# Kernel optimization log

Measured on AMD Instinct MI355X. Metric: run time of the kernel, lower is better.

The kernel has to match this reference:

```python
import jax, jax.numpy as jnp
from jax import lax
import numpy as np

KERNEL_SIZE = 29
N_T = 1000
SIGMA_MIN, SIGMA_MAX = 0.5, 20.0
HIDDEN = 32


def _gaussian_kernel1d(sigma, ksize):
    # torchvision: linspace over [-half, half], normalized gaussian pdf
    half = (ksize - 1) * 0.5
    xg = jnp.linspace(-half, half, ksize)
    pdf = jnp.exp(-0.5 * (xg / sigma) ** 2)
    return pdf / pdf.sum()


def batch_blur(x, sigmas, ksize=KERNEL_SIZE):
    # x: [B,C,H,W], sigmas: [B]. Per-sample separable gaussian blur as a single
    # grouped depthwise conv (feature_group_count = B*C) instead of a Python loop.
    B, C, H, W = x.shape
    k1 = jax.vmap(lambda s: _gaussian_kernel1d(s, ksize))(sigmas)  # [B, k]
    pad = ksize // 2
    xp = jnp.pad(x, ((0, 0), (0, 0), (pad, pad), (pad, pad)), mode='reflect')
    lhs = xp.reshape(1, B * C, H + 2 * pad, W + 2 * pad)
    kbc = jnp.repeat(k1, C, axis=0)  # [B*C, k] per-channel kernel
    # vertical pass then horizontal pass (outer-product 2D kernel == two 1D passes)
    y = lax.conv_general_dilated(lhs, kbc[:, None, :, None], (1, 1), 'VALID',
                                 feature_group_count=B * C)
    y = lax.conv_general_dilated(y, kbc[:, None, None, :], (1, 1), 'VALID',
                                 feature_group_count=B * C)
    return y.reshape(B, C, H, W)


def gt_net(z, tn, W1, b1, tw, W2, b2):
    # simple time-conditioned conv net standing in for the opaque `gt` module
    h = lax.conv_general_dilated(z, W1, (1, 1), 'SAME')  # [B,HIDDEN,H,W]
    h = h + b1[None, :, None, None] + (tn[:, None] * tw[None, :])[:, :, None, None]
    h = jax.nn.relu(h)
    out = lax.conv_general_dilated(h, W2, (1, 1), 'SAME') + b2[None, :, None, None]
    return out


def setup_inputs() -> dict:
    key = jax.random.key(0)
    ks = jax.random.split(key, 6)
    B, C, H, W = 32, 3, 256, 256
    x = jax.random.normal(ks[0], (B, C, H, W), dtype=jnp.float32)
    t = jax.random.randint(ks[1], (B,), 0, N_T, dtype=jnp.int32)
    W1 = jax.random.normal(ks[2], (HIDDEN, C, 3, 3), dtype=jnp.float32) * 0.1
    b1 = jnp.zeros((HIDDEN,), dtype=jnp.float32)
    tw = jax.random.normal(ks[3], (HIDDEN,), dtype=jnp.float32) * 0.1
    W2 = jax.random.normal(ks[4], (C, HIDDEN, 3, 3), dtype=jnp.float32) * 0.1
    b2 = jnp.zeros((C,), dtype=jnp.float32)
    sigma_schedule = jnp.linspace(SIGMA_MIN, SIGMA_MAX, N_T, dtype=jnp.float32)
    return {"x": x, "t": t, "W1": W1, "b1": b1, "tw": tw, "W2": W2, "b2": b2,
            "sigma_schedule": sigma_schedule}


def reference(x, t, W1, b1, tw, W2, b2, sigma_schedule):
    sigma_t = sigma_schedule[t]                      # [B]
    z_t = batch_blur(x, sigma_t, KERNEL_SIZE)        # [B,C,H,W]
    preds = gt_net(z_t, t.astype(jnp.float32) / N_T, W1, b1, tw, W2, b2)
    return jnp.mean((x - preds) ** 2)                # MSELoss
```

## Files before the change

### kernel.cpp

```cpp
#include <hip/hip_runtime.h>
#include <hip/hip_bf16.h>

#define BATCH 32
#define CH 3
#define HH 256
#define WW 256
#define KS 29
#define PAD 14
#define NT_F 1000.0f

#define RB 16

typedef __attribute__((ext_vector_type(8))) short short8;
typedef __attribute__((ext_vector_type(4))) float f32x4;
typedef __attribute__((ext_vector_type(16))) float f32x16;

union U4 { short8 s8; uint4 u4; };

__device__ inline unsigned short bf16rne(float f) {
  unsigned u = __float_as_uint(f);
  unsigned r = (u + 0x7FFFu + ((u >> 16) & 1u)) >> 16;
  return (unsigned short)r;
}
__device__ inline unsigned pk_bf16(float a, float b) {
  union { __hip_bfloat162 h2; unsigned u; } cv;
  cv.h2 = __float22bfloat162_rn(make_float2(a, b));
  return cv.u;
}


#define PARTIAL_OFF 3151872

__global__ __launch_bounds__(256, 4) void blur_kernel(
    const float* __restrict__ x, const int* __restrict__ t,
    const float* __restrict__ sched, const float* __restrict__ W1,
    const float* __restrict__ b1, const float* __restrict__ tw,
    const float* __restrict__ W2, float* __restrict__ ws,
    unsigned short* __restrict__ z) {
  int blk = blockIdx.x;
  int tid = threadIdx.x;

  if (blk >= BATCH * CH * RB) {
    float* tcond = ws + 1024;
    unsigned short* w1n = (unsigned short*)(ws + 2048);
    unsigned short* w2c = (unsigned short*)(ws + 2816);
    for (int i = tid; i < 1536; i += 256) {
      int mf = i >> 9, r = i & 511;
      int och = r >> 4, s = r & 15;
      int tp = mf * 4 + (s >> 2), ci = s & 3;
      w1n[i] = (ci < 3 && tp < 9) ? bf16rne(W1[och * 27 + ci * 9 + tp])
                                  : (unsigned short)0;
    }
    for (int i = tid; i < 4608; i += 256) {
      int tap = i >> 9, r = i & 511;
      int n = r >> 5, s = r & 31;
      int och = (s & 3) + 8 * ((s >> 2) & 3) + 4 * (s >> 4);
      int dy = tap / 3, dx = tap - dy * 3;
      w2c[i] = (n < 3) ? bf16rne(W2[((n * 32 + och) * 3 + dy) * 3 + dx])
                       : (unsigned short)0;
    }
    for (int i = tid; i < 1024; i += 256) {
      int b = i >> 5, o = i & 31;
      tcond[i] = b1[o] + ((float)t[b] * (1.0f / NT_F)) * tw[o];
    }
    return;
  }

  {
    int wid = (blk & 7) * 192 + (blk >> 3);
    blk = wid;
  }

  __shared__ float vsp[RB][288];
  __shared__ float gkl[32];
  int rg = blk & (RB - 1);
  int bc = blk >> 4;
  int b = bc / CH;
  int y0 = rg * RB;
  const float* xp = x + (size_t)bc * (HH * WW);

  if (tid < 64) {
    float wexp = 0.0f;
    if (tid < KS) {
      float sigma = sched[t[b]];
      float xg = (float)(tid - PAD) / sigma;
      wexp = expf(-0.5f * xg * xg);
    }
    float s = wexp;
#pragma unroll
    for (int off = 32; off > 0; off >>= 1) s += __shfl_down(s, off);
    float tot = __shfl(s, 0);
    if (tid < 32) gkl[tid] = wexp / tot;
  }
  __syncthreads();

  float gk[KS];
#pragma unroll
  for (int kk = 0; kk < KS; kk++) gk[kk] = gkl[kk];

#pragma unroll
  for (int ch = 0; ch < 2; ch++) {
    float acc[8];
#pragma unroll
    for (int yy = 0; yy < 8; yy++) acc[yy] = 0.0f;
#pragma unroll
    for (int i = 0; i < 36; i++) {
      int gy = y0 + 8 * ch - PAD + i;
      gy = (gy < 0) ? -gy : gy;
      gy = (gy >= HH) ? (2 * HH - 2 - gy) : gy;
      float v = xp[gy * WW + tid];
#pragma unroll
      for (int yy = 0; yy < 8; yy++) {
        int kk = i - yy;
        if (kk >= 0 && kk < KS) acc[yy] += gk[kk] * v;
      }
    }
#pragma unroll
    for (int yy = 0; yy < 8; yy++) vsp[8 * ch + yy][tid + 16] = acc[yy];
  }
  __syncthreads();
  {
    int row = tid >> 4, i2 = tid & 15;
    vsp[row][i2] = vsp[row][32 - i2];
    vsp[row][272 + i2] = vsp[row][270 - i2];
  }
  __syncthreads();

  size_t zb = (size_t)bc * (HH * WW);
#pragma unroll
  for (int it = 0; it < RB / 4; ++it) {
    int unit = tid + 256 * it;
    int row = unit >> 6, cg = unit & 63;
    float w[36];
#pragma unroll
    for (int i = 0; i < 9; i++)
      *(float4*)&w[4 * i] = *(const float4*)&vsp[row][4 * (cg + i)];
    float o0 = 0, o1 = 0, o2 = 0, o3 = 0;
#pragma unroll
    for (int kk = 0; kk < KS; kk++) {
      float kv = gk[kk];
      o0 += kv * w[2 + kk];
      o1 += kv * w[3 + kk];
      o2 += kv * w[4 + kk];
      o3 += kv * w[5 + kk];
    }
    unsigned u0 = pk_bf16(o0, o1);
    unsigned u1 = pk_bf16(o2, o3);
    *(uint2*)&z[zb + (size_t)(y0 + row) * WW + 4 * cg] = make_uint2(u0, u1);
  }
}

__global__ __launch_bounds__(256, 5) void convloss_kernel(
    const float* __restrict__ x, const float* __restrict__ ws,
    const float* __restrict__ b2g, float* __restrict__ partial) {
  __shared__ __align__(16) unsigned short zs4[400 * 4];
  __shared__ __align__(16) unsigned short hsw[4 * 6 * 18 * 32];
  __shared__ float wsum[4];

  const float* tcond = ws + 1024;
  const unsigned short* w1n = (const unsigned short*)(ws + 2048);
  const unsigned short* w2c = (const unsigned short*)(ws + 2816);
  const unsigned short* zg = (const unsigned short*)(ws + 5120);

  int flat = (blockIdx.z * 16 + blockIdx.y) * 16 + blockIdx.x;
  int wid = (flat & 7) * 1024 + (flat >> 3);
  int b = wid >> 8;
  int by = (wid >> 4) & 15;
  int bx = wid & 15;

  int tid = threadIdx.x;
  int x0 = bx * 16, y0 = by * 16;
  const unsigned short* zbp = zg + (size_t)b * 3 * HH * WW;

  int lane = tid & 63;
  int q = lane >> 4;
  int col = lane & 15;
  int col32 = lane & 31;
  int h = lane >> 5;
  int wv = tid >> 6;

  if (tid < 200) {
    int zy = tid / 10;
    int zx2 = tid - zy * 10;
    int gy = y0 - 2 + zy;
    int gx0 = x0 - 2 + 2 * zx2;
    bool ok = ((unsigned)gy < (unsigned)HH) && ((unsigned)gx0 < (unsigned)(WW - 1));
    int cy = (gy < 0) ? 0 : ((gy > 255) ? 255 : gy);
    int cx = (gx0 < 0) ? 0 : ((gx0 > 254) ? 254 : gx0);
    int gi = cy * WW + cx;
    unsigned c0 = *(const unsigned*)&zbp[gi];
    unsigned c1 = *(const unsigned*)&zbp[HH * WW + gi];
    unsigned c2 = *(const unsigned*)&zbp[2 * HH * WW + gi];
    unsigned m = ok ? 0xFFFFFFFFu : 0u;
    c0 &= m; c1 &= m; c2 &= m;
    uint4 o;
    o.x = (c0 & 0xFFFFu) | (c1 << 16);
    o.y = c2 & 0xFFFFu;
    o.z = (c0 >> 16) | (c1 & 0xFFFF0000u);
    o.w = c2 >> 16;
    *(uint4*)&zs4[(zy * 20 + 2 * zx2) * 4] = o;
  }

  U4 W0, W1f, W2f;
  W0.u4  = *(const uint4*)(w1n + 0 * 512 + col32 * 16 + h * 8);
  W1f.u4 = *(const uint4*)(w1n + 1 * 512 + col32 * 16 + h * 8);
  W2f.u4 = *(const uint4*)(w1n + 2 * 512 + col32 * 16 + h * 8);

  f32x16 tc16;
#pragma unroll
  for (int r1 = 0; r1 < 4; r1++) {
    float4 v = *(const float4*)(tcond + b * 32 + 4 * h + 8 * r1);
    tc16[4 * r1 + 0] = v.x;
    tc16[4 * r1 + 1] = v.y;
    tc16[4 * r1 + 2] = v.z;
    tc16[4 * r1 + 3] = v.w;
  }

  int colc = (col < 3) ? col : 0;
  float b2v = b2g[colc];

  const float* xb = x + (size_t)b * 3 * HH * WW;
  float4 xpre[4];
#pragma unroll
  for (int i = 0; i < 4; i++) {
    int g2 = wv * 4 + i;
    xpre[i] = *(const float4*)&xb[colc * (HH * WW) + (y0 + g2) * WW + x0 + q * 4];
  }

  __syncthreads();

  int oA0 = h ? 8 : 0, oB0 = h ? 80 : 4;
  int oA1 = h ? 160 : 84, oB1 = h ? 164 : 88;
  const int oA2 = 168;

  char* hbw = (char*)hsw + wv * 6912;
#pragma unroll
  for (int g2 = 0; g2 < 4; g2++) {
    int e = g2 * 32 + col32;
    int ec = (e > 107) ? 107 : e;
    int row_l = ec / 18;
    int px = ec - row_l * 18;
    int ub = ((4 * wv + row_l) * 20 + px) * 4;
    uint2 l0 = *(const uint2*)&zs4[ub + oA0];
    uint2 l1 = *(const uint2*)&zs4[ub + oB0];
    uint2 l2 = *(const uint2*)&zs4[ub + oA1];
    uint2 l3 = *(const uint2*)&zs4[ub + oB1];
    uint2 l4 = *(const uint2*)&zs4[ub + oA2];
    U4 Bz0, Bz1, Bz2;
    Bz0.u4 = make_uint4(l0.x, l0.y, l1.x, l1.y);
    Bz1.u4 = make_uint4(l2.x, l2.y, l3.x, l3.y);
    Bz2.u4 = make_uint4(l4.x, l4.y, 0u, 0u);
    f32x16 a = __builtin_amdgcn_mfma_f32_32x32x16_bf16(W0.s8, Bz0.s8, tc16, 0, 0, 0);
    a = __builtin_amdgcn_mfma_f32_32x32x16_bf16(W1f.s8, Bz1.s8, a, 0, 0, 0);
    a = __builtin_amdgcn_mfma_f32_32x32x16_bf16(W2f.s8, Bz2.s8, a, 0, 0, 0);
    if (e < 108) {
      unsigned wpk[8];
#pragma unroll
      for (int m = 0; m < 8; m++)
        wpk[m] = pk_bf16(fmaxf(a[2 * m], 0.0f), fmaxf(a[2 * m + 1], 0.0f));
      int wb = row_l * 1152 + px * 64 + ((32 * h) ^ ((px & 2) << 4));
      *(uint4*)(hbw + wb)      = make_uint4(wpk[0], wpk[1], wpk[2], wpk[3]);
      *(uint4*)(hbw + wb + 16) = make_uint4(wpk[4], wpk[5], wpk[6], wpk[7]);
    }
  }

  U4 Bt[3][3];
  {
    const unsigned short* wbase = w2c + col * 32 + q * 8;
#pragma unroll
    for (int dy = 0; dy < 3; dy++)
#pragma unroll
      for (int dx = 0; dx < 3; dx++)
        Bt[dy][dx].u4 = *(const uint4*)(wbase + (dy * 3 + dx) * 512);
  }

  const f32x4 bcv = {b2v, b2v, b2v, b2v};
  f32x4 dacc[4];
#pragma unroll
  for (int i = 0; i < 4; i++) dacc[i] = bcv;
  {
    const char* hb = (const char*)hsw + wv * 6912;
#pragma unroll
    for (int dx = 0; dx < 3; dx++) {
      int px = col + dx;
      const char* bp = hb + px * 64 + ((q * 16) ^ ((px & 2) << 4));
#pragma unroll
      for (int rr = 0; rr < 6; rr++) {
        U4 A;
        A.u4 = *(const uint4*)(bp + rr * 1152);
        if (rr < 4)
          dacc[rr] = __builtin_amdgcn_mfma_f32_16x16x32_bf16(A.s8, Bt[0][dx].s8, dacc[rr], 0, 0, 0);
        if (rr >= 1 && rr < 5)
          dacc[rr - 1] = __builtin_amdgcn_mfma_f32_16x16x32_bf16(A.s8, Bt[1][dx].s8, dacc[rr - 1], 0, 0, 0);
        if (rr >= 2)
          dacc[rr - 2] = __builtin_amdgcn_mfma_f32_16x16x32_bf16(A.s8, Bt[2][dx].s8, dacc[rr - 2], 0, 0, 0);
      }
    }
  }

  float s = 0.0f;
  if (col < 3) {
#pragma unroll
    for (int i = 0; i < 4; i++) {
      float4 xv = xpre[i];
      float d0 = xv.x - dacc[i][0];
      float d1 = xv.y - dacc[i][1];
      float d2 = xv.z - dacc[i][2];
      float d3 = xv.w - dacc[i][3];
      s += d0 * d0 + d1 * d1 + d2 * d2 + d3 * d3;
    }
  }
#pragma unroll
  for (int off = 32; off > 0; off >>= 1) s += __shfl_down(s, off);
  if (lane == 0) wsum[wv] = s;
  __syncthreads();
  if (tid == 0) {
    int bid = (b * 16 + by) * 16 + bx;
    partial[bid] = wsum[0] + wsum[1] + wsum[2] + wsum[3];
  }
}

__global__ __launch_bounds__(256) void reduce_kernel(const float* __restrict__ partial,
                                                     float* __restrict__ out) {
  __shared__ float wsum[4];
  int tid = threadIdx.x;
  float s = 0.0f;
#pragma unroll
  for (int i = 0; i < 8; i++) {
    float4 v = *(const float4*)&partial[(tid + 256 * i) * 4];
    s += v.x + v.y + v.z + v.w;
  }
#pragma unroll
  for (int off = 32; off > 0; off >>= 1) s += __shfl_down(s, off);
  if ((tid & 63) == 0) wsum[tid >> 6] = s;
  __syncthreads();
  if (tid == 0)
    out[0] = (wsum[0] + wsum[1] + wsum[2] + wsum[3]) * (1.0f / 6291456.0f);
}

extern "C" void kernel_launch(void* const* d_in, const int* in_sizes, int n_in,
                              void* d_out, int out_size, void* d_ws, size_t ws_size,
                              hipStream_t stream) {
  const float* x = (const float*)d_in[0];
  const int* t = (const int*)d_in[1];
  const float* W1 = (const float*)d_in[2];
  const float* b1 = (const float*)d_in[3];
  const float* tw = (const float*)d_in[4];
  const float* W2 = (const float*)d_in[5];
  const float* b2 = (const float*)d_in[6];
  const float* sched = (const float*)d_in[7];
  float* out = (float*)d_out;
  float* ws = (float*)d_ws;
  unsigned short* z = (unsigned short*)(ws + 5120);
  float* partial = ws + PARTIAL_OFF;

  blur_kernel<<<BATCH * CH * RB + 1, 256, 0, stream>>>(x, t, sched, W1, b1, tw, W2, ws, z);
  dim3 grid(16, 16, BATCH);
  convloss_kernel<<<grid, 256, 0, stream>>>(x, ws, b2, partial);
  reduce_kernel<<<1, 256, 0, stream>>>(partial, out);
}
```

Before: 134.5 us.

## Process two tiles per convloss block with prefetched second z tile

Each convloss block now handles two adjacent 16x16 tiles, halving the grid. The second tile's z values and x inputs are loaded into registers while the first tile runs its MFMA convolutions, then written to a second shared buffer. The intent is to hide global-load latency and amortise per-block setup such as weight loads and the final reduction. In exchange it uses more registers and shared memory, lowers the occupancy hint from 5 to 4, and the reduce kernel reads half as many partials.

```diff
diff --git a/kernel.cpp b/kernel.cpp
--- a/kernel.cpp
+++ b/kernel.cpp
@@ -150,10 +150,11 @@
   }
 }
 
-__global__ __launch_bounds__(256, 5) void convloss_kernel(
+__global__ __launch_bounds__(256, 4) void convloss_kernel(
     const float* __restrict__ x, const float* __restrict__ ws,
     const float* __restrict__ b2g, float* __restrict__ partial) {
-  __shared__ __align__(16) unsigned short zs4[400 * 4];
+  __shared__ __align__(16) unsigned short zsA[400 * 4];
+  __shared__ __align__(16) unsigned short zsB[400 * 4];
   __shared__ __align__(16) unsigned short hsw[4 * 6 * 18 * 32];
   __shared__ float wsum[4];
 
@@ -162,14 +163,15 @@
   const unsigned short* w2c = (const unsigned short*)(ws + 2816);
   const unsigned short* zg = (const unsigned short*)(ws + 5120);
 
-  int flat = (blockIdx.z * 16 + blockIdx.y) * 16 + blockIdx.x;
-  int wid = (flat & 7) * 1024 + (flat >> 3);
-  int b = wid >> 8;
-  int by = (wid >> 4) & 15;
-  int bx = wid & 15;
+  int flat = (blockIdx.z * 16 + blockIdx.y) * 8 + blockIdx.x;
+  int wid = (flat & 7) * 512 + (flat >> 3);
+  int b = wid >> 7;
+  int by = (wid >> 3) & 15;
+  int bxp = wid & 7;
 
   int tid = threadIdx.x;
-  int x0 = bx * 16, y0 = by * 16;
+  int x0a = bxp * 32, x0b = x0a + 16;
+  int y0 = by * 16;
   const unsigned short* zbp = zg + (size_t)b * 3 * HH * WW;
 
   int lane = tid & 63;
@@ -179,26 +181,39 @@
   int h = lane >> 5;
   int wv = tid >> 6;
 
-  if (tid < 200) {
-    int zy = tid / 10;
-    int zx2 = tid - zy * 10;
+  int colc = (col < 3) ? col : 0;
+  float b2v = b2g[colc];
+  const float* xb = x + (size_t)b * 3 * HH * WW;
+
+  int zy = tid / 10;
+  int zx2 = tid - zy * 10;
+
+  auto stage_load = [&](int x0t, unsigned& c0, unsigned& c1, unsigned& c2) {
     int gy = y0 - 2 + zy;
-    int gx0 = x0 - 2 + 2 * zx2;
+    int gx0 = x0t - 2 + 2 * zx2;
     bool ok = ((unsigned)gy < (unsigned)HH) && ((unsigned)gx0 < (unsigned)(WW - 1));
     int cy = (gy < 0) ? 0 : ((gy > 255) ? 255 : gy);
     int cx = (gx0 < 0) ? 0 : ((gx0 > 254) ? 254 : gx0);
     int gi = cy * WW + cx;
-    unsigned c0 = *(const unsigned*)&zbp[gi];
-    unsigned c1 = *(const unsigned*)&zbp[HH * WW + gi];
-    unsigned c2 = *(const unsigned*)&zbp[2 * HH * WW + gi];
+    c0 = *(const unsigned*)&zbp[gi];
+    c1 = *(const unsigned*)&zbp[HH * WW + gi];
+    c2 = *(const unsigned*)&zbp[2 * HH * WW + gi];
     unsigned m = ok ? 0xFFFFFFFFu : 0u;
     c0 &= m; c1 &= m; c2 &= m;
+  };
+  auto stage_write = [&](unsigned c0, unsigned c1, unsigned c2, unsigned short* zs) {
     uint4 o;
     o.x = (c0 & 0xFFFFu) | (c1 << 16);
     o.y = c2 & 0xFFFFu;
     o.z = (c0 >> 16) | (c1 & 0xFFFF0000u);
     o.w = c2 >> 16;
-    *(uint4*)&zs4[(zy * 20 + 2 * zx2) * 4] = o;
+    *(uint4*)&zs[(zy * 20 + 2 * zx2) * 4] = o;
+  };
+
+  if (tid < 200) {
+    unsigned c0, c1, c2;
+    stage_load(x0a, c0, c1, c2);
+    stage_write(c0, c1, c2, zsA);
   }
 
   U4 W0, W1f, W2f;
@@ -216,74 +231,78 @@
     tc16[4 * r1 + 3] = v.w;
   }
 
-  int colc = (col < 3) ? col : 0;
-  float b2v = b2g[colc];
-
-  const float* xb = x + (size_t)b * 3 * HH * WW;
-  float4 xpre[4];
+  float4 xpreA[4];
 #pragma unroll
   for (int i = 0; i < 4; i++) {
     int g2 = wv * 4 + i;
-    xpre[i] = *(const float4*)&xb[colc * (HH * WW) + (y0 + g2) * WW + x0 + q * 4];
-  }
-
-  __syncthreads();
+    xpreA[i] = *(const float4*)&xb[colc * (HH * WW) + (y0 + g2) * WW + x0a + q * 4];
+  }
+
+  __syncthreads();
+
+  unsigned s0b = 0, s1b = 0, s2b = 0;
+  if (tid < 200) stage_load(x0b, s0b, s1b, s2b);
+  float4 xpreB[4];
+#pragma unroll
+  for (int i = 0; i < 4; i++) {
+    int g2 = wv * 4 + i;
+    xpreB[i] = *(const float4*)&xb[colc * (HH * WW) + (y0 + g2) * WW + x0b + q * 4];
+  }
 
   int oA0 = h ? 8 : 0, oB0 = h ? 80 : 4;
   int oA1 = h ? 160 : 84, oB1 = h ? 164 : 88;
   const int oA2 = 168;
-
   char* hbw = (char*)hsw + wv * 6912;
-#pragma unroll
-  for (int g2 = 0; g2 < 4; g2++) {
-    int e = g2 * 32 + col32;
-    int ec = (e > 107) ? 107 : e;
-    int row_l = ec / 18;
-    int px = ec - row_l * 18;
-    int ub = ((4 * wv + row_l) * 20 + px) * 4;
-    uint2 l0 = *(const uint2*)&zs4[ub + oA0];
-    uint2 l1 = *(const uint2*)&zs4[ub + oB0];
-    uint2 l2 = *(const uint2*)&zs4[ub + oA1];
-    uint2 l3 = *(const uint2*)&zs4[ub + oB1];
-    uint2 l4 = *(const uint2*)&zs4[ub + oA2];
-    U4 Bz0, Bz1, Bz2;
-    Bz0.u4 = make_uint4(l0.x, l0.y, l1.x, l1.y);
-    Bz1.u4 = make_uint4(l2.x, l2.y, l3.x, l3.y);
-    Bz2.u4 = make_uint4(l4.x, l4.y, 0u, 0u);
-    f32x16 a = __builtin_amdgcn_mfma_f32_32x32x16_bf16(W0.s8, Bz0.s8, tc16, 0, 0, 0);
-    a = __builtin_amdgcn_mfma_f32_32x32x16_bf16(W1f.s8, Bz1.s8, a, 0, 0, 0);
-    a = __builtin_amdgcn_mfma_f32_32x32x16_bf16(W2f.s8, Bz2.s8, a, 0, 0, 0);
-    if (e < 108) {
-      unsigned wpk[8];
-#pragma unroll
-      for (int m = 0; m < 8; m++)
-        wpk[m] = pk_bf16(fmaxf(a[2 * m], 0.0f), fmaxf(a[2 * m + 1], 0.0f));
-      int wb = row_l * 1152 + px * 64 + ((32 * h) ^ ((px & 2) << 4));
-      *(uint4*)(hbw + wb)      = make_uint4(wpk[0], wpk[1], wpk[2], wpk[3]);
-      *(uint4*)(hbw + wb + 16) = make_uint4(wpk[4], wpk[5], wpk[6], wpk[7]);
-    }
-  }
-
-  U4 Bt[3][3];
-  {
-    const unsigned short* wbase = w2c + col * 32 + q * 8;
-#pragma unroll
-    for (int dy = 0; dy < 3; dy++)
-#pragma unroll
-      for (int dx = 0; dx < 3; dx++)
-        Bt[dy][dx].u4 = *(const uint4*)(wbase + (dy * 3 + dx) * 512);
-  }
-
-  const f32x4 bcv = {b2v, b2v, b2v, b2v};
-  f32x4 dacc[4];
-#pragma unroll
-  for (int i = 0; i < 4; i++) dacc[i] = bcv;
-  {
-    const char* hb = (const char*)hsw + wv * 6912;
+
+  auto conv_tile = [&](const unsigned short* zs, const float4* xp) -> float {
+#pragma unroll
+    for (int g2 = 0; g2 < 4; g2++) {
+      int e = g2 * 32 + col32;
+      int ec = (e > 107) ? 107 : e;
+      int row_l = ec / 18;
+      int px = ec - row_l * 18;
+      int ub = ((4 * wv + row_l) * 20 + px) * 4;
+      uint2 l0 = *(const uint2*)&zs[ub + oA0];
+      uint2 l1 = *(const uint2*)&zs[ub + oB0];
+      uint2 l2 = *(const uint2*)&zs[ub + oA1];
+      uint2 l3 = *(const uint2*)&zs[ub + oB1];
+      uint2 l4 = *(const uint2*)&zs[ub + oA2];
+      U4 Bz0, Bz1, Bz2;
+      Bz0.u4 = make_uint4(l0.x, l0.y, l1.x, l1.y);
+      Bz1.u4 = make_uint4(l2.x, l2.y, l3.x, l3.y);
+      Bz2.u4 = make_uint4(l4.x, l4.y, 0u, 0u);
+      f32x16 a = __builtin_amdgcn_mfma_f32_32x32x16_bf16(W0.s8, Bz0.s8, tc16, 0, 0, 0);
+      a = __builtin_amdgcn_mfma_f32_32x32x16_bf16(W1f.s8, Bz1.s8, a, 0, 0, 0);
+      a = __builtin_amdgcn_mfma_f32_32x32x16_bf16(W2f.s8, Bz2.s8, a, 0, 0, 0);
+      if (e < 108) {
+        unsigned wpk[8];
+#pragma unroll
+        for (int m = 0; m < 8; m++)
+          wpk[m] = pk_bf16(fmaxf(a[2 * m], 0.0f), fmaxf(a[2 * m + 1], 0.0f));
+        int wb = row_l * 1152 + px * 64 + ((32 * h) ^ ((px & 2) << 4));
+        *(uint4*)(hbw + wb)      = make_uint4(wpk[0], wpk[1], wpk[2], wpk[3]);
+        *(uint4*)(hbw + wb + 16) = make_uint4(wpk[4], wpk[5], wpk[6], wpk[7]);
+      }
+    }
+
+    U4 Bt[3][3];
+    {
+      const unsigned short* wbase = w2c + col * 32 + q * 8;
+#pragma unroll
+      for (int dy = 0; dy < 3; dy++)
+#pragma unroll
+        for (int dx = 0; dx < 3; dx++)
+          Bt[dy][dx].u4 = *(const uint4*)(wbase + (dy * 3 + dx) * 512);
+    }
+
+    const f32x4 bcv = {b2v, b2v, b2v, b2v};
+    f32x4 dacc[4];
+#pragma unroll
+    for (int i = 0; i < 4; i++) dacc[i] = bcv;
 #pragma unroll
     for (int dx = 0; dx < 3; dx++) {
       int px = col + dx;
-      const char* bp = hb + px * 64 + ((q * 16) ^ ((px & 2) << 4));
+      const char* bp = (const char*)hbw + px * 64 + ((q * 16) ^ ((px & 2) << 4));
 #pragma unroll
       for (int rr = 0; rr < 6; rr++) {
         U4 A;
@@ -296,26 +315,35 @@
           dacc[rr - 2] = __builtin_amdgcn_mfma_f32_16x16x32_bf16(A.s8, Bt[2][dx].s8, dacc[rr - 2], 0, 0, 0);
       }
     }
-  }
-
-  float s = 0.0f;
-  if (col < 3) {
-#pragma unroll
-    for (int i = 0; i < 4; i++) {
-      float4 xv = xpre[i];
-      float d0 = xv.x - dacc[i][0];
-      float d1 = xv.y - dacc[i][1];
-      float d2 = xv.z - dacc[i][2];
-      float d3 = xv.w - dacc[i][3];
-      s += d0 * d0 + d1 * d1 + d2 * d2 + d3 * d3;
-    }
-  }
-#pragma unroll
-  for (int off = 32; off > 0; off >>= 1) s += __shfl_down(s, off);
-  if (lane == 0) wsum[wv] = s;
+
+    float s = 0.0f;
+    if (col < 3) {
+#pragma unroll
+      for (int i = 0; i < 4; i++) {
+        float4 xv = xp[i];
+        float d0 = xv.x - dacc[i][0];
+        float d1 = xv.y - dacc[i][1];
+        float d2 = xv.z - dacc[i][2];
+        float d3 = xv.w - dacc[i][3];
+        s += d0 * d0 + d1 * d1 + d2 * d2 + d3 * d3;
+      }
+    }
+    return s;
+  };
+
+  float sacc = conv_tile(zsA, xpreA);
+
+  if (tid < 200) stage_write(s0b, s1b, s2b, zsB);
+  __syncthreads();
+
+  sacc += conv_tile(zsB, xpreB);
+
+#pragma unroll
+  for (int off = 32; off > 0; off >>= 1) sacc += __shfl_down(sacc, off);
+  if (lane == 0) wsum[wv] = sacc;
   __syncthreads();
   if (tid == 0) {
-    int bid = (b * 16 + by) * 16 + bx;
+    int bid = (b * 16 + by) * 8 + bxp;
     partial[bid] = wsum[0] + wsum[1] + wsum[2] + wsum[3];
   }
 }
@@ -326,7 +354,7 @@
   int tid = threadIdx.x;
   float s = 0.0f;
 #pragma unroll
-  for (int i = 0; i < 8; i++) {
+  for (int i = 0; i < 4; i++) {
     float4 v = *(const float4*)&partial[(tid + 256 * i) * 4];
     s += v.x + v.y + v.z + v.w;
   }
@@ -355,7 +383,7 @@
   float* partial = ws + PARTIAL_OFF;
 
   blur_kernel<<<BATCH * CH * RB + 1, 256, 0, stream>>>(x, t, sched, W1, b1, tw, W2, ws, z);
-  dim3 grid(16, 16, BATCH);
+  dim3 grid(8, 16, BATCH);
   convloss_kernel<<<grid, 256, 0, stream>>>(x, ws, b2, partial);
   reduce_kernel<<<1, 256, 0, stream>>>(partial, out);
 }
```

New measurement: 152.5 us. 1.13x slower.
